# Optimization experiments

Measured on AMD Instinct MI355X. Metric: run time of the kernel, lower is better.

The kernel has to match this reference:

```python
import jax, jax.numpy as jnp
import numpy as np

TOP_K = 2  # MoE top-k routing


def setup_inputs() -> dict:
    key = jax.random.key(0)
    ks = jax.random.split(key, 5)
    B, D, H, O, N = 8192, 3072, 128, 10, 8
    scale_g = 1.0 / np.sqrt(D)
    return {
        "x": jax.random.normal(ks[0], (B, D), dtype=jnp.float32),
        "Wg": jax.random.normal(ks[1], (D, N), dtype=jnp.float32) * scale_g,
        "bg": jnp.zeros((N,), dtype=jnp.float32),
        "W1": jax.random.normal(ks[2], (N, D, H), dtype=jnp.float32) * scale_g,
        "b1": jnp.zeros((N, H), dtype=jnp.float32),
        "W2": jax.random.normal(ks[3], (N, H, O), dtype=jnp.float32) * (1.0 / np.sqrt(H)),
        "b2": jnp.zeros((N, O), dtype=jnp.float32),
    }


def reference(x, Wg, bg, W1, b1, W2, b2):
    # Gating: logits -> top-k -> softmax over the k selected logits
    g = x @ Wg + bg                                  # [B, N]
    tv, ti = jax.lax.top_k(g, TOP_K)                 # [B, k]
    w = jax.nn.softmax(tv, axis=-1)                  # [B, k]
    # Expert MLPs, computed densely over all experts (vectorized dispatch)
    h = jax.nn.relu(jnp.einsum('bd,edh->beh', x, W1) + b1)   # [B, N, H]
    y = jnp.einsum('beh,eho->beo', h, W2) + b2               # [B, N, O]
    # Combine: gather each token's k selected expert outputs, weight, sum
    ysel = jnp.take_along_axis(y, ti[:, :, None], axis=1)    # [B, k, O]
    return jnp.sum(w[:, :, None] * ysel, axis=1)             # [B, O]
```

## Files before the change

### kernel.cpp

```cpp
#include <hip/hip_runtime.h>
#include <hip/hip_bf16.h>

#define B_TOK 8192
#define D_DIM 3072
#define H_DIM 128
#define O_DIM 10
#define N_EXP 8

#define BM 128
#define BK2 128
#define HLDS_STRIDE 136
#define CHK 768
#define NCHK 4
#define ESTRIDE 4096

typedef __bf16 bf16x8 __attribute__((ext_vector_type(8)));
typedef float  f32x4  __attribute__((ext_vector_type(4)));
typedef unsigned short us8 __attribute__((ext_vector_type(8)));

__device__ __forceinline__ unsigned short f2bf(float f) {
  unsigned int u = __float_as_uint(f);
  unsigned int r = (u + 0x7FFFu + ((u >> 16) & 1u)) >> 16;
  return (unsigned short)r;
}

__device__ __forceinline__ void async16(const void* g, void* l) {
  __builtin_amdgcn_global_load_lds(
      (const __attribute__((address_space(1))) void*)g,
      (__attribute__((address_space(3))) void*)l,
      16, 0, 0);
}

__global__ __launch_bounds__(256) void k0_w1_transpose(const float* __restrict__ W1,
                                                       unsigned short* __restrict__ w1t) {
  __shared__ __align__(16) unsigned short lds[64 * 72];
  const int e  = blockIdx.z;
  const int d0 = blockIdx.x * 64;
  const int h0 = blockIdx.y * 64;
  const int tid = threadIdx.x;

  const float* src = W1 + ((size_t)e * D_DIM + d0) * H_DIM + h0;
  const int hl = tid & 63;
  const int dg = tid >> 6;
#pragma unroll
  for (int k = 0; k < 16; ++k) {
    const int d = dg + 4 * k;
    lds[hl * 72 + d] = f2bf(src[(size_t)d * H_DIM + hl]);
  }
  __syncthreads();

  unsigned short* dst = w1t + ((size_t)e * H_DIM + h0) * D_DIM + d0;
  const int q  = tid & 7;
  const int h1 = tid >> 3;
#pragma unroll
  for (int k = 0; k < 2; ++k) {
    const int h = h1 + 32 * k;
    const int d = q * 8;
    us8 v = *(const us8*)(lds + h * 72 + d);
    *(us8*)(dst + (size_t)h * D_DIM + d) = v;
  }
}

__global__ __launch_bounds__(256) void k1a_stream(
    const float* __restrict__ x, const float* __restrict__ Wg,
    unsigned short* __restrict__ xb, float* __restrict__ gpart) {
  __shared__ float wg_lds[N_EXP * CHK];
  const int c   = blockIdx.y;
  const int d0  = c * CHK;
  const int tid = threadIdx.x;

  for (int f = tid; f < CHK * N_EXP / 4; f += 256) {
    const float4 v = ((const float4*)(Wg + (size_t)d0 * N_EXP))[f];
    const int dl = f >> 1;
    const int nh = (f & 1) * 4;
    wg_lds[(nh + 0) * CHK + dl] = v.x;
    wg_lds[(nh + 1) * CHK + dl] = v.y;
    wg_lds[(nh + 2) * CHK + dl] = v.z;
    wg_lds[(nh + 3) * CHK + dl] = v.w;
  }
  __syncthreads();

  const int lane = tid & 63;
  const int wv   = tid >> 6;
  const int t0   = blockIdx.x * 16 + wv * 4;

  const float* xr0 = x + (size_t)(t0 + 0) * D_DIM + d0;
  const float* xr1 = x + (size_t)(t0 + 1) * D_DIM + d0;
  const float* xr2 = x + (size_t)(t0 + 2) * D_DIM + d0;
  const float* xr3 = x + (size_t)(t0 + 3) * D_DIM + d0;
  unsigned short* xw0 = xb + (size_t)(t0 + 0) * D_DIM + d0;
  unsigned short* xw1 = xb + (size_t)(t0 + 1) * D_DIM + d0;
  unsigned short* xw2 = xb + (size_t)(t0 + 2) * D_DIM + d0;
  unsigned short* xw3 = xb + (size_t)(t0 + 3) * D_DIM + d0;

  float acc[4][N_EXP];
#pragma unroll
  for (int t = 0; t < 4; ++t)
#pragma unroll
    for (int n = 0; n < N_EXP; ++n) acc[t][n] = 0.f;

#pragma unroll
  for (int s = 0; s < CHK / 256; ++s) {
    const int dl = s * 256 + lane * 4;
    float4 xv0 = *(const float4*)(xr0 + dl);
    float4 xv1 = *(const float4*)(xr1 + dl);
    float4 xv2 = *(const float4*)(xr2 + dl);
    float4 xv3 = *(const float4*)(xr3 + dl);
    float4 w4[N_EXP];
#pragma unroll
    for (int n = 0; n < N_EXP; ++n)
      w4[n] = *(const float4*)(wg_lds + n * CHK + dl);
    ushort4 p;
    p.x = f2bf(xv0.x); p.y = f2bf(xv0.y); p.z = f2bf(xv0.z); p.w = f2bf(xv0.w);
    *(ushort4*)(xw0 + dl) = p;
    p.x = f2bf(xv1.x); p.y = f2bf(xv1.y); p.z = f2bf(xv1.z); p.w = f2bf(xv1.w);
    *(ushort4*)(xw1 + dl) = p;
    p.x = f2bf(xv2.x); p.y = f2bf(xv2.y); p.z = f2bf(xv2.z); p.w = f2bf(xv2.w);
    *(ushort4*)(xw2 + dl) = p;
    p.x = f2bf(xv3.x); p.y = f2bf(xv3.y); p.z = f2bf(xv3.z); p.w = f2bf(xv3.w);
    *(ushort4*)(xw3 + dl) = p;
#pragma unroll
    for (int n = 0; n < N_EXP; ++n) {
      acc[0][n] = fmaf(xv0.x, w4[n].x, acc[0][n]);
      acc[0][n] = fmaf(xv0.y, w4[n].y, acc[0][n]);
      acc[0][n] = fmaf(xv0.z, w4[n].z, acc[0][n]);
      acc[0][n] = fmaf(xv0.w, w4[n].w, acc[0][n]);
      acc[1][n] = fmaf(xv1.x, w4[n].x, acc[1][n]);
      acc[1][n] = fmaf(xv1.y, w4[n].y, acc[1][n]);
      acc[1][n] = fmaf(xv1.z, w4[n].z, acc[1][n]);
      acc[1][n] = fmaf(xv1.w, w4[n].w, acc[1][n]);
      acc[2][n] = fmaf(xv2.x, w4[n].x, acc[2][n]);
      acc[2][n] = fmaf(xv2.y, w4[n].y, acc[2][n]);
      acc[2][n] = fmaf(xv2.z, w4[n].z, acc[2][n]);
      acc[2][n] = fmaf(xv2.w, w4[n].w, acc[2][n]);
      acc[3][n] = fmaf(xv3.x, w4[n].x, acc[3][n]);
      acc[3][n] = fmaf(xv3.y, w4[n].y, acc[3][n]);
      acc[3][n] = fmaf(xv3.z, w4[n].z, acc[3][n]);
      acc[3][n] = fmaf(xv3.w, w4[n].w, acc[3][n]);
    }
  }

#pragma unroll
  for (int t = 0; t < 4; ++t)
#pragma unroll
    for (int n = 0; n < N_EXP; ++n) {
#pragma unroll
      for (int off = 32; off > 0; off >>= 1)
        acc[t][n] += __shfl_xor(acc[t][n], off, 64);
    }
  if (lane == 0) {
#pragma unroll
    for (int t = 0; t < 4; ++t) {
      float* gp = gpart + ((size_t)c * B_TOK + (t0 + t)) * N_EXP;
      *(float4*)(gp)     = make_float4(acc[t][0], acc[t][1], acc[t][2], acc[t][3]);
      *(float4*)(gp + 4) = make_float4(acc[t][4], acc[t][5], acc[t][6], acc[t][7]);
    }
  }
}

__global__ __launch_bounds__(256) void k1c_topk(
    const float* __restrict__ gpart, const float* __restrict__ bg,
    int4* __restrict__ idx4, float2* __restrict__ wts, int* __restrict__ cnt,
    int* __restrict__ tlist) {
  __shared__ int lcnt[N_EXP], gbase[N_EXP];
  __shared__ float bgs[N_EXP];
  const int tid = threadIdx.x;
  if (tid < N_EXP) { lcnt[tid] = 0; bgs[tid] = bg[tid]; }
  __syncthreads();
  const int t = blockIdx.x * 256 + tid;

  float g[N_EXP];
#pragma unroll
  for (int n = 0; n < N_EXP; ++n) g[n] = bgs[n];
#pragma unroll
  for (int c = 0; c < NCHK; ++c) {
    const float* gp = gpart + ((size_t)c * B_TOK + t) * N_EXP;
    float4 a = *(const float4*)(gp);
    float4 b = *(const float4*)(gp + 4);
    g[0] += a.x; g[1] += a.y; g[2] += a.z; g[3] += a.w;
    g[4] += b.x; g[5] += b.y; g[6] += b.z; g[7] += b.w;
  }
  int i0 = 0;
#pragma unroll
  for (int n = 1; n < N_EXP; ++n) if (g[n] > g[i0]) i0 = n;
  int i1 = (i0 == 0) ? 1 : 0;
#pragma unroll
  for (int n = 0; n < N_EXP; ++n) if (n != i0 && g[n] > g[i1]) i1 = n;
  const float e1 = expf(g[i1] - g[i0]);
  const float inv = 1.f / (1.f + e1);
  const int lp0 = atomicAdd(&lcnt[i0], 1);
  const int lp1 = atomicAdd(&lcnt[i1], 1);
  __syncthreads();
  if (tid < N_EXP) gbase[tid] = atomicAdd(&cnt[tid], lcnt[tid]);
  __syncthreads();
  int p0 = gbase[i0] + lp0; p0 = p0 < ESTRIDE ? p0 : ESTRIDE - 1;
  int p1 = gbase[i1] + lp1; p1 = p1 < ESTRIDE ? p1 : ESTRIDE - 1;
  tlist[i0 * ESTRIDE + p0] = t;
  tlist[i1 * ESTRIDE + p1] = t;
  idx4[t] = make_int4(i0, p0, i1, p1);
  wts[t]  = make_float2(inv, e1 * inv);
}

__global__ __launch_bounds__(256) void k2_experts(
    const unsigned short* __restrict__ xb,
    const unsigned short* __restrict__ w1t,
    const float* __restrict__ b1,
    const float* __restrict__ W2,
    const float* __restrict__ b2,
    const int* __restrict__ cnt, const int* __restrict__ tlist,
    float* __restrict__ ypair) {
  const int e    = blockIdx.y;
  int n_e        = cnt[e];
  n_e            = n_e < ESTRIDE ? n_e : ESTRIDE;
  const int row0 = blockIdx.x * BM;
  if (row0 >= n_e) return;

  __shared__ __align__(16) unsigned short sm[65536 + 2048];
  unsigned short* h_lds   = sm;
  unsigned short* w2t_lds = sm + 65536;

  const int tid  = threadIdx.x;
  const int lane = tid & 63;
  const int wv   = tid >> 6;
  const int quad = lane >> 4;
  const int cl   = lane & 15;

  const unsigned short* Abase[8];
  const unsigned short* Bbase[8];
#pragma unroll
  for (int j = 0; j < 8; ++j) {
    const int rloc = wv * 32 + j * 4 + quad;
    int gr = row0 + rloc;
    gr = gr < n_e ? gr : n_e - 1;
    const int koff = ((cl - (j * 4 + quad)) & 15) * 8;
    Abase[j] = xb + (size_t)tlist[e * ESTRIDE + gr] * D_DIM + koff;
    Bbase[j] = w1t + ((size_t)e * H_DIM + rloc) * D_DIM + koff;
  }

#define STAGE(it, pp)                                                     \
  {                                                                       \
    const int ko = (it) * BK2;                                            \
    unsigned short* abuf = sm + (pp) * 32768;                             \
    unsigned short* bbuf = sm + 16384 + (pp) * 32768;                     \
    _Pragma("unroll")                                                     \
    for (int j = 0; j < 8; ++j) {                                         \
      const int ldsrow = (wv * 32 + j * 4) * BK2;                         \
      async16(Abase[j] + ko, abuf + ldsrow);                              \
      async16(Bbase[j] + ko, bbuf + ldsrow);                              \
    }                                                                     \
  }

  STAGE(0, 0);

  const float* W2e = W2 + (size_t)e * H_DIM * O_DIM;
  for (int idx = tid; idx < 16 * 128; idx += 256) {
    const int o = idx >> 7, hh = idx & 127;
    const float v = (o < O_DIM) ? W2e[hh * O_DIM + o] : 0.f;
    w2t_lds[o * 128 + ((((hh >> 3) + o) & 15) * 8) + (hh & 7)] = f2bf(v);
  }

  const int mhalf = (wv >> 1) * 64;
  const int nhalf = (wv & 1) * 64;

  f32x4 acc[4][4];
#pragma unroll
  for (int i = 0; i < 4; ++i)
#pragma unroll
    for (int j = 0; j < 4; ++j)
      acc[i][j] = (f32x4){0.f, 0.f, 0.f, 0.f};

  const int NIT = D_DIM / BK2;
  for (int it = 0; it < NIT; ++it) {
    __syncthreads();
    if (it + 1 < NIT) STAGE(it + 1, (it + 1) & 1);
    const unsigned short* al = sm + (it & 1) * 32768;
    const unsigned short* bl = sm + 16384 + (it & 1) * 32768;
#pragma unroll
    for (int kk = 0; kk < 4; ++kk) {
      const int pos = ((kk * 4 + quad + cl) & 15) * 8;
      bf16x8 af[4], bfr[4];
#pragma unroll
      for (int mi = 0; mi < 4; ++mi)
        af[mi] = *(const bf16x8*)(al + (mhalf + mi * 16 + cl) * BK2 + pos);
#pragma unroll
      for (int ni = 0; ni < 4; ++ni)
        bfr[ni] = *(const bf16x8*)(bl + (nhalf + ni * 16 + cl) * BK2 + pos);
#pragma unroll
      for (int mi = 0; mi < 4; ++mi)
#pragma unroll
        for (int ni = 0; ni < 4; ++ni)
          acc[mi][ni] = __builtin_amdgcn_mfma_f32_16x16x32_bf16(af[mi], bfr[ni], acc[mi][ni], 0, 0, 0);
    }
  }
  __syncthreads();

  const float* b1e = b1 + e * H_DIM;
#pragma unroll
  for (int ni = 0; ni < 4; ++ni) {
    const int col  = nhalf + ni * 16 + cl;
    const float bias = b1e[col];
#pragma unroll
    for (int mi = 0; mi < 4; ++mi) {
      const int rbase = mhalf + mi * 16 + (quad << 2);
#pragma unroll
      for (int r = 0; r < 4; ++r) {
        float v = acc[mi][ni][r] + bias;
        v = v > 0.f ? v : 0.f;
        h_lds[(rbase + r) * HLDS_STRIDE + col] = f2bf(v);
      }
    }
  }
  __syncthreads();

  f32x4 acc2[2];
  acc2[0] = (f32x4){0.f, 0.f, 0.f, 0.f};
  acc2[1] = (f32x4){0.f, 0.f, 0.f, 0.f};
#pragma unroll
  for (int ks = 0; ks < 4; ++ks) {
    const int krd = ks * 32 + quad * 8;
    bf16x8 bfr = *(const bf16x8*)(w2t_lds + cl * 128 + ((ks * 4 + quad + cl) & 15) * 8);
#pragma unroll
    for (int mi = 0; mi < 2; ++mi) {
      bf16x8 afr = *(const bf16x8*)(h_lds + (wv * 32 + mi * 16 + cl) * HLDS_STRIDE + krd);
      acc2[mi] = __builtin_amdgcn_mfma_f32_16x16x32_bf16(afr, bfr, acc2[mi], 0, 0, 0);
    }
  }
  const int o = cl;
  if (o < O_DIM) {
    const float bias2 = b2[e * O_DIM + o];
#pragma unroll
    for (int mi = 0; mi < 2; ++mi) {
#pragma unroll
      for (int r = 0; r < 4; ++r) {
        const int rl = wv * 32 + mi * 16 + (quad << 2) + r;
        if (row0 + rl < n_e)
          ypair[(size_t)(e * ESTRIDE + row0 + rl) * 16 + o] = acc2[mi][r] + bias2;
      }
    }
  }
}

__global__ __launch_bounds__(256) void k3_combine(
    const float* __restrict__ ypair, const int4* __restrict__ idx4,
    const float2* __restrict__ wts, float* __restrict__ out) {
  const int g = blockIdx.x * 256 + threadIdx.x;
  if (g >= B_TOK * O_DIM) return;
  const int b = g / O_DIM, o = g - b * O_DIM;
  const int4 r = idx4[b];
  const float2 w = wts[b];
  out[g] = w.x * ypair[(size_t)(r.x * ESTRIDE + r.y) * 16 + o] +
           w.y * ypair[(size_t)(r.z * ESTRIDE + r.w) * 16 + o];
}

extern "C" void kernel_launch(void* const* d_in, const int* in_sizes, int n_in,
                              void* d_out, int out_size, void* d_ws, size_t ws_size,
                              hipStream_t stream) {
  const float* x  = (const float*)d_in[0];
  const float* Wg = (const float*)d_in[1];
  const float* bg = (const float*)d_in[2];
  const float* W1 = (const float*)d_in[3];
  const float* b1 = (const float*)d_in[4];
  const float* W2 = (const float*)d_in[5];
  const float* b2 = (const float*)d_in[6];
  float* out = (float*)d_out;

  char* ws = (char*)d_ws;
  unsigned short* xb  = (unsigned short*)ws;
  unsigned short* w1t = (unsigned short*)(ws + 50331648);
  int4*   idx4  = (int4*)  (ws + 56623104);
  float2* wts   = (float2*)(ws + 56754176);
  int*    cnt   = (int*)   (ws + 56819712);
  int*    tlist = (int*)   (ws + 56819840);
  float*  gpart = (float*) (ws + 56950912);
  float*  ypair = (float*) (ws + 56950912);

  k0_w1_transpose<<<dim3(48, 2, 8), dim3(256), 0, stream>>>(W1, w1t);
  (void)hipMemsetAsync(cnt, 0, N_EXP * sizeof(int), stream);
  k1a_stream<<<dim3(B_TOK / 16, NCHK), dim3(256), 0, stream>>>(x, Wg, xb, gpart);
  k1c_topk<<<dim3(B_TOK / 256), dim3(256), 0, stream>>>(gpart, bg, idx4, wts, cnt, tlist);
  k2_experts<<<dim3(ESTRIDE / BM, N_EXP), dim3(256), 0, stream>>>(
      xb, w1t, b1, W2, b2, cnt, tlist, ypair);
  k3_combine<<<dim3((B_TOK * O_DIM + 255) / 256), dim3(256), 0, stream>>>(
      ypair, idx4, wts, out);
}
```

Baseline: 233.0 us.

## Fuse W1 transpose with gating stream and scatter-combine via atomics in expert kernel

Merges the W1 bf16 transpose and the x-conversion/gating-partial kernels into one launch, splitting work by block index, with each gating block now handling 32 tokens. It also drops the separate combine kernel: top-k writes per-slot routing weights, and the expert kernel atomically adds weighted outputs straight into a zeroed output buffer. The aim is to cut launch count, the ypair round trip and tail idle time. The cost is an extra memset, float atomics with nondeterministic summation order, and a heavier branching fused kernel.

```diff
diff --git a/kernel.cpp b/kernel.cpp
--- a/kernel.cpp
+++ b/kernel.cpp
@@ -14,6 +14,9 @@
 #define NCHK 4
 #define ESTRIDE 4096
 
+#define K1A_BLOCKS 1024
+#define K0_BLOCKS  768
+
 typedef __bf16 bf16x8 __attribute__((ext_vector_type(8)));
 typedef float  f32x4  __attribute__((ext_vector_type(4)));
 typedef unsigned short us8 __attribute__((ext_vector_type(8)));
@@ -31,43 +34,48 @@
       16, 0, 0);
 }
 
-__global__ __launch_bounds__(256) void k0_w1_transpose(const float* __restrict__ W1,
-                                                       unsigned short* __restrict__ w1t) {
-  __shared__ __align__(16) unsigned short lds[64 * 72];
-  const int e  = blockIdx.z;
-  const int d0 = blockIdx.x * 64;
-  const int h0 = blockIdx.y * 64;
+__global__ __launch_bounds__(256, 4) void k01_fused(
+    const float* __restrict__ x, const float* __restrict__ Wg,
+    unsigned short* __restrict__ xb, float* __restrict__ gpart,
+    const float* __restrict__ W1, unsigned short* __restrict__ w1t) {
+  __shared__ __align__(16) char smem[N_EXP * CHK * 4];
   const int tid = threadIdx.x;
 
-  const float* src = W1 + ((size_t)e * D_DIM + d0) * H_DIM + h0;
-  const int hl = tid & 63;
-  const int dg = tid >> 6;
-#pragma unroll
-  for (int k = 0; k < 16; ++k) {
-    const int d = dg + 4 * k;
-    lds[hl * 72 + d] = f2bf(src[(size_t)d * H_DIM + hl]);
-  }
-  __syncthreads();
-
-  unsigned short* dst = w1t + ((size_t)e * H_DIM + h0) * D_DIM + d0;
-  const int q  = tid & 7;
-  const int h1 = tid >> 3;
-#pragma unroll
-  for (int k = 0; k < 2; ++k) {
-    const int h = h1 + 32 * k;
-    const int d = q * 8;
-    us8 v = *(const us8*)(lds + h * 72 + d);
-    *(us8*)(dst + (size_t)h * D_DIM + d) = v;
-  }
-}
-
-__global__ __launch_bounds__(256) void k1a_stream(
-    const float* __restrict__ x, const float* __restrict__ Wg,
-    unsigned short* __restrict__ xb, float* __restrict__ gpart) {
-  __shared__ float wg_lds[N_EXP * CHK];
-  const int c   = blockIdx.y;
-  const int d0  = c * CHK;
-  const int tid = threadIdx.x;
+  if (blockIdx.x >= K1A_BLOCKS) {
+    unsigned short* lds = (unsigned short*)smem;
+    const int id = blockIdx.x - K1A_BLOCKS;
+    const int e  = id / 96;
+    const int r  = id - e * 96;
+    const int h0 = (r / 48) * 64;
+    const int d0 = (r % 48) * 64;
+
+    const float* src = W1 + ((size_t)e * D_DIM + d0) * H_DIM + h0;
+    const int hl = tid & 63;
+    const int dg = tid >> 6;
+#pragma unroll
+    for (int k = 0; k < 16; ++k) {
+      const int d = dg + 4 * k;
+      lds[hl * 72 + d] = f2bf(src[(size_t)d * H_DIM + hl]);
+    }
+    __syncthreads();
+
+    unsigned short* dst = w1t + ((size_t)e * H_DIM + h0) * D_DIM + d0;
+    const int q  = tid & 7;
+    const int h1 = tid >> 3;
+#pragma unroll
+    for (int k = 0; k < 2; ++k) {
+      const int h = h1 + 32 * k;
+      const int d = q * 8;
+      us8 v = *(const us8*)(lds + h * 72 + d);
+      *(us8*)(dst + (size_t)h * D_DIM + d) = v;
+    }
+    return;
+  }
+
+  float* wg_lds = (float*)smem;
+  const int c  = blockIdx.x >> 8;
+  const int bx = blockIdx.x & 255;
+  const int d0 = c * CHK;
 
   for (int f = tid; f < CHK * N_EXP / 4; f += 256) {
     const float4 v = ((const float4*)(Wg + (size_t)d0 * N_EXP))[f];
@@ -82,86 +90,88 @@
 
   const int lane = tid & 63;
   const int wv   = tid >> 6;
-  const int t0   = blockIdx.x * 16 + wv * 4;
-
-  const float* xr0 = x + (size_t)(t0 + 0) * D_DIM + d0;
-  const float* xr1 = x + (size_t)(t0 + 1) * D_DIM + d0;
-  const float* xr2 = x + (size_t)(t0 + 2) * D_DIM + d0;
-  const float* xr3 = x + (size_t)(t0 + 3) * D_DIM + d0;
-  unsigned short* xw0 = xb + (size_t)(t0 + 0) * D_DIM + d0;
-  unsigned short* xw1 = xb + (size_t)(t0 + 1) * D_DIM + d0;
-  unsigned short* xw2 = xb + (size_t)(t0 + 2) * D_DIM + d0;
-  unsigned short* xw3 = xb + (size_t)(t0 + 3) * D_DIM + d0;
-
-  float acc[4][N_EXP];
-#pragma unroll
-  for (int t = 0; t < 4; ++t)
-#pragma unroll
-    for (int n = 0; n < N_EXP; ++n) acc[t][n] = 0.f;
-
-#pragma unroll
-  for (int s = 0; s < CHK / 256; ++s) {
-    const int dl = s * 256 + lane * 4;
-    float4 xv0 = *(const float4*)(xr0 + dl);
-    float4 xv1 = *(const float4*)(xr1 + dl);
-    float4 xv2 = *(const float4*)(xr2 + dl);
-    float4 xv3 = *(const float4*)(xr3 + dl);
-    float4 w4[N_EXP];
-#pragma unroll
-    for (int n = 0; n < N_EXP; ++n)
-      w4[n] = *(const float4*)(wg_lds + n * CHK + dl);
-    ushort4 p;
-    p.x = f2bf(xv0.x); p.y = f2bf(xv0.y); p.z = f2bf(xv0.z); p.w = f2bf(xv0.w);
-    *(ushort4*)(xw0 + dl) = p;
-    p.x = f2bf(xv1.x); p.y = f2bf(xv1.y); p.z = f2bf(xv1.z); p.w = f2bf(xv1.w);
-    *(ushort4*)(xw1 + dl) = p;
-    p.x = f2bf(xv2.x); p.y = f2bf(xv2.y); p.z = f2bf(xv2.z); p.w = f2bf(xv2.w);
-    *(ushort4*)(xw2 + dl) = p;
-    p.x = f2bf(xv3.x); p.y = f2bf(xv3.y); p.z = f2bf(xv3.z); p.w = f2bf(xv3.w);
-    *(ushort4*)(xw3 + dl) = p;
-#pragma unroll
-    for (int n = 0; n < N_EXP; ++n) {
-      acc[0][n] = fmaf(xv0.x, w4[n].x, acc[0][n]);
-      acc[0][n] = fmaf(xv0.y, w4[n].y, acc[0][n]);
-      acc[0][n] = fmaf(xv0.z, w4[n].z, acc[0][n]);
-      acc[0][n] = fmaf(xv0.w, w4[n].w, acc[0][n]);
-      acc[1][n] = fmaf(xv1.x, w4[n].x, acc[1][n]);
-      acc[1][n] = fmaf(xv1.y, w4[n].y, acc[1][n]);
-      acc[1][n] = fmaf(xv1.z, w4[n].z, acc[1][n]);
-      acc[1][n] = fmaf(xv1.w, w4[n].w, acc[1][n]);
-      acc[2][n] = fmaf(xv2.x, w4[n].x, acc[2][n]);
-      acc[2][n] = fmaf(xv2.y, w4[n].y, acc[2][n]);
-      acc[2][n] = fmaf(xv2.z, w4[n].z, acc[2][n]);
-      acc[2][n] = fmaf(xv2.w, w4[n].w, acc[2][n]);
-      acc[3][n] = fmaf(xv3.x, w4[n].x, acc[3][n]);
-      acc[3][n] = fmaf(xv3.y, w4[n].y, acc[3][n]);
-      acc[3][n] = fmaf(xv3.z, w4[n].z, acc[3][n]);
-      acc[3][n] = fmaf(xv3.w, w4[n].w, acc[3][n]);
-    }
-  }
-
-#pragma unroll
-  for (int t = 0; t < 4; ++t)
-#pragma unroll
-    for (int n = 0; n < N_EXP; ++n) {
-#pragma unroll
-      for (int off = 32; off > 0; off >>= 1)
-        acc[t][n] += __shfl_xor(acc[t][n], off, 64);
-    }
-  if (lane == 0) {
-#pragma unroll
-    for (int t = 0; t < 4; ++t) {
-      float* gp = gpart + ((size_t)c * B_TOK + (t0 + t)) * N_EXP;
-      *(float4*)(gp)     = make_float4(acc[t][0], acc[t][1], acc[t][2], acc[t][3]);
-      *(float4*)(gp + 4) = make_float4(acc[t][4], acc[t][5], acc[t][6], acc[t][7]);
+
+  for (int g = 0; g < 2; ++g) {
+    const int t0 = bx * 32 + g * 16 + wv * 4;
+
+    const float* xr0 = x + (size_t)(t0 + 0) * D_DIM + d0;
+    const float* xr1 = x + (size_t)(t0 + 1) * D_DIM + d0;
+    const float* xr2 = x + (size_t)(t0 + 2) * D_DIM + d0;
+    const float* xr3 = x + (size_t)(t0 + 3) * D_DIM + d0;
+    unsigned short* xw0 = xb + (size_t)(t0 + 0) * D_DIM + d0;
+    unsigned short* xw1 = xb + (size_t)(t0 + 1) * D_DIM + d0;
+    unsigned short* xw2 = xb + (size_t)(t0 + 2) * D_DIM + d0;
+    unsigned short* xw3 = xb + (size_t)(t0 + 3) * D_DIM + d0;
+
+    float acc[4][N_EXP];
+#pragma unroll
+    for (int t = 0; t < 4; ++t)
+#pragma unroll
+      for (int n = 0; n < N_EXP; ++n) acc[t][n] = 0.f;
+
+#pragma unroll
+    for (int s = 0; s < CHK / 256; ++s) {
+      const int dl = s * 256 + lane * 4;
+      float4 xv0 = *(const float4*)(xr0 + dl);
+      float4 xv1 = *(const float4*)(xr1 + dl);
+      float4 xv2 = *(const float4*)(xr2 + dl);
+      float4 xv3 = *(const float4*)(xr3 + dl);
+      float4 w4[N_EXP];
+#pragma unroll
+      for (int n = 0; n < N_EXP; ++n)
+        w4[n] = *(const float4*)(wg_lds + n * CHK + dl);
+      ushort4 p;
+      p.x = f2bf(xv0.x); p.y = f2bf(xv0.y); p.z = f2bf(xv0.z); p.w = f2bf(xv0.w);
+      *(ushort4*)(xw0 + dl) = p;
+      p.x = f2bf(xv1.x); p.y = f2bf(xv1.y); p.z = f2bf(xv1.z); p.w = f2bf(xv1.w);
+      *(ushort4*)(xw1 + dl) = p;
+      p.x = f2bf(xv2.x); p.y = f2bf(xv2.y); p.z = f2bf(xv2.z); p.w = f2bf(xv2.w);
+      *(ushort4*)(xw2 + dl) = p;
+      p.x = f2bf(xv3.x); p.y = f2bf(xv3.y); p.z = f2bf(xv3.z); p.w = f2bf(xv3.w);
+      *(ushort4*)(xw3 + dl) = p;
+#pragma unroll
+      for (int n = 0; n < N_EXP; ++n) {
+        acc[0][n] = fmaf(xv0.x, w4[n].x, acc[0][n]);
+        acc[0][n] = fmaf(xv0.y, w4[n].y, acc[0][n]);
+        acc[0][n] = fmaf(xv0.z, w4[n].z, acc[0][n]);
+        acc[0][n] = fmaf(xv0.w, w4[n].w, acc[0][n]);
+        acc[1][n] = fmaf(xv1.x, w4[n].x, acc[1][n]);
+        acc[1][n] = fmaf(xv1.y, w4[n].y, acc[1][n]);
+        acc[1][n] = fmaf(xv1.z, w4[n].z, acc[1][n]);
+        acc[1][n] = fmaf(xv1.w, w4[n].w, acc[1][n]);
+        acc[2][n] = fmaf(xv2.x, w4[n].x, acc[2][n]);
+        acc[2][n] = fmaf(xv2.y, w4[n].y, acc[2][n]);
+        acc[2][n] = fmaf(xv2.z, w4[n].z, acc[2][n]);
+        acc[2][n] = fmaf(xv2.w, w4[n].w, acc[2][n]);
+        acc[3][n] = fmaf(xv3.x, w4[n].x, acc[3][n]);
+        acc[3][n] = fmaf(xv3.y, w4[n].y, acc[3][n]);
+        acc[3][n] = fmaf(xv3.z, w4[n].z, acc[3][n]);
+        acc[3][n] = fmaf(xv3.w, w4[n].w, acc[3][n]);
+      }
+    }
+
+#pragma unroll
+    for (int t = 0; t < 4; ++t)
+#pragma unroll
+      for (int n = 0; n < N_EXP; ++n) {
+#pragma unroll
+        for (int off = 32; off > 0; off >>= 1)
+          acc[t][n] += __shfl_xor(acc[t][n], off, 64);
+      }
+    if (lane == 0) {
+#pragma unroll
+      for (int t = 0; t < 4; ++t) {
+        float* gp = gpart + ((size_t)c * B_TOK + (t0 + t)) * N_EXP;
+        *(float4*)(gp)     = make_float4(acc[t][0], acc[t][1], acc[t][2], acc[t][3]);
+        *(float4*)(gp + 4) = make_float4(acc[t][4], acc[t][5], acc[t][6], acc[t][7]);
+      }
     }
   }
 }
 
 __global__ __launch_bounds__(256) void k1c_topk(
     const float* __restrict__ gpart, const float* __restrict__ bg,
-    int4* __restrict__ idx4, float2* __restrict__ wts, int* __restrict__ cnt,
-    int* __restrict__ tlist) {
+    int* __restrict__ cnt, int* __restrict__ tlist, float* __restrict__ wslot) {
   __shared__ int lcnt[N_EXP], gbase[N_EXP];
   __shared__ float bgs[N_EXP];
   const int tid = threadIdx.x;
@@ -197,8 +207,8 @@
   int p1 = gbase[i1] + lp1; p1 = p1 < ESTRIDE ? p1 : ESTRIDE - 1;
   tlist[i0 * ESTRIDE + p0] = t;
   tlist[i1 * ESTRIDE + p1] = t;
-  idx4[t] = make_int4(i0, p0, i1, p1);
-  wts[t]  = make_float2(inv, e1 * inv);
+  wslot[i0 * ESTRIDE + p0] = inv;
+  wslot[i1 * ESTRIDE + p1] = e1 * inv;
 }
 
 __global__ __launch_bounds__(256) void k2_experts(
@@ -208,7 +218,8 @@
     const float* __restrict__ W2,
     const float* __restrict__ b2,
     const int* __restrict__ cnt, const int* __restrict__ tlist,
-    float* __restrict__ ypair) {
+    const float* __restrict__ wslot,
+    float* __restrict__ out) {
   const int e    = blockIdx.y;
   int n_e        = cnt[e];
   n_e            = n_e < ESTRIDE ? n_e : ESTRIDE;
@@ -333,23 +344,15 @@
 #pragma unroll
       for (int r = 0; r < 4; ++r) {
         const int rl = wv * 32 + mi * 16 + (quad << 2) + r;
-        if (row0 + rl < n_e)
-          ypair[(size_t)(e * ESTRIDE + row0 + rl) * 16 + o] = acc2[mi][r] + bias2;
-      }
-    }
-  }
-}
-
-__global__ __launch_bounds__(256) void k3_combine(
-    const float* __restrict__ ypair, const int4* __restrict__ idx4,
-    const float2* __restrict__ wts, float* __restrict__ out) {
-  const int g = blockIdx.x * 256 + threadIdx.x;
-  if (g >= B_TOK * O_DIM) return;
-  const int b = g / O_DIM, o = g - b * O_DIM;
-  const int4 r = idx4[b];
-  const float2 w = wts[b];
-  out[g] = w.x * ypair[(size_t)(r.x * ESTRIDE + r.y) * 16 + o] +
-           w.y * ypair[(size_t)(r.z * ESTRIDE + r.w) * 16 + o];
+        const int slot = row0 + rl;
+        if (slot < n_e) {
+          const int t = tlist[e * ESTRIDE + slot];
+          const float w = wslot[e * ESTRIDE + slot];
+          atomicAdd(out + (size_t)t * O_DIM + o, w * (acc2[mi][r] + bias2));
+        }
+      }
+    }
+  }
 }
 
 extern "C" void kernel_launch(void* const* d_in, const int* in_sizes, int n_in,
@@ -367,19 +370,16 @@
   char* ws = (char*)d_ws;
   unsigned short* xb  = (unsigned short*)ws;
   unsigned short* w1t = (unsigned short*)(ws + 50331648);
-  int4*   idx4  = (int4*)  (ws + 56623104);
-  float2* wts   = (float2*)(ws + 56754176);
-  int*    cnt   = (int*)   (ws + 56819712);
-  int*    tlist = (int*)   (ws + 56819840);
-  float*  gpart = (float*) (ws + 56950912);
-  float*  ypair = (float*) (ws + 56950912);
-
-  k0_w1_transpose<<<dim3(48, 2, 8), dim3(256), 0, stream>>>(W1, w1t);
+  int*    cnt   = (int*)   (ws + 56623104);
+  int*    tlist = (int*)   (ws + 56623232);
+  float*  wslot = (float*) (ws + 56754304);
+  float*  gpart = (float*) (ws + 56885376);
+
   (void)hipMemsetAsync(cnt, 0, N_EXP * sizeof(int), stream);
-  k1a_stream<<<dim3(B_TOK / 16, NCHK), dim3(256), 0, stream>>>(x, Wg, xb, gpart);
-  k1c_topk<<<dim3(B_TOK / 256), dim3(256), 0, stream>>>(gpart, bg, idx4, wts, cnt, tlist);
+  (void)hipMemsetAsync(out, 0, (size_t)B_TOK * O_DIM * sizeof(float), stream);
+  k01_fused<<<dim3(K1A_BLOCKS + K0_BLOCKS), dim3(256), 0, stream>>>(
+      x, Wg, xb, gpart, W1, w1t);
+  k1c_topk<<<dim3(B_TOK / 256), dim3(256), 0, stream>>>(gpart, bg, cnt, tlist, wslot);
   k2_experts<<<dim3(ESTRIDE / BM, N_EXP), dim3(256), 0, stream>>>(
-      xb, w1t, b1, W2, b2, cnt, tlist, ypair);
-  k3_combine<<<dim3((B_TOK * O_DIM + 255) / 256), dim3(256), 0, stream>>>(
-      ypair, idx4, wts, out);
-}
+      xb, w1t, b1, W2, b2, cnt, tlist, wslot, out);
+}
```

Result: slower. 298.5 us (+28.1%).
